# Kernel optimization log

Hardware: AMD Instinct MI355X
Metric: run time of the kernel (lower is better)

Reference implementation:

```python
import jax, jax.numpy as jnp
import numpy as np

B, S, E = 2, 2048, 1024
H = 16
D = E // H          # head_dim = 64
W = 32              # sliding window / block size


def setup_inputs() -> dict:
    key = jax.random.key(0)
    k1, k2, k3 = jax.random.split(key, 3)
    x = jax.random.normal(k1, (B, S, E), dtype=jnp.float32)
    # xavier-uniform-like scale for the projections
    lim_qkv = float(np.sqrt(6.0 / (E + 3 * E)))
    lim_o = float(np.sqrt(6.0 / (E + E)))
    Wqkv = jax.random.uniform(k2, (3 * E, E), minval=-lim_qkv, maxval=lim_qkv, dtype=jnp.float32)
    bqkv = jnp.zeros((3 * E,), dtype=jnp.float32)
    Wo = jax.random.uniform(k3, (E, E), minval=-lim_o, maxval=lim_o, dtype=jnp.float32)
    bo = jnp.zeros((E,), dtype=jnp.float32)
    return {"x": x, "Wqkv": Wqkv, "bqkv": bqkv, "Wo": Wo, "bo": bo}


def _roll_blocks(kb, w):
    # kb: (BH, nb, w, d). Replicates roll(): w circularly-shifted copies along the
    # block axis, original inserted at index (w-1)//2, concatenated within-block.
    shifts = list(range(1, w))
    shifts.insert((w - 1) // 2, 0)
    return jnp.concatenate([jnp.roll(kb, s, axis=1) for s in shifts], axis=2)  # (BH, nb, w*w, d)


def reference(x, Wqkv, bqkv, Wo, bo):
    b, s, e = x.shape
    qkv = x @ Wqkv.T + bqkv                              # (B,S,3E)
    qkv = qkv.reshape(b, s, H, 3 * D).transpose(0, 2, 1, 3)  # (B,H,S,3D)
    q, k, v = jnp.split(qkv, 3, axis=-1)                 # each (B,H,S,D)

    nb = s // W
    qb = q.reshape(b * H, nb, W, D)
    kb = k.reshape(b * H, nb, W, D)
    kblk = _roll_blocks(kb, W)                           # (BH, nb, W*W, D)
    qk = jnp.einsum('bcxd,bcyd->bcxy', qb, kblk)         # (BH, nb, W, W*W)
    attn = qk.reshape(b, H, s, W * W) / jnp.sqrt(jnp.float32(D))
    attn = jax.nn.softmax(attn, axis=-1)
    # Faithful to torch.einsum('ijkl,ijkm->ijkm', attn, v): sum attn over its
    # last axis (==1 after softmax) and broadcast-multiply v.
    vals = attn.sum(axis=-1, keepdims=True) * v          # (B,H,S,D)

    vals = vals.transpose(0, 2, 1, 3).reshape(b, s, e)   # (B,S,E)
    return vals @ Wo.T + bo
```

## Files before the change

kernel.cpp:

```cpp
#include <hip/hip_runtime.h>
#include <hip/hip_bf16.h>
#include <type_traits>

#define MROWS 4096
#define EDIM  1024

typedef __attribute__((ext_vector_type(8))) __bf16 bf16x8;
typedef __attribute__((ext_vector_type(4))) float f32x4;
typedef __attribute__((ext_vector_type(8))) unsigned short ushort8;
typedef __attribute__((ext_vector_type(4))) unsigned short ushort4v;

__device__ __forceinline__ unsigned short f2bf(float f) {
    unsigned u = __builtin_bit_cast(unsigned, f);
    u += 0x7FFFu + ((u >> 16) & 1u);
    return (unsigned short)(u >> 16);
}

__device__ __forceinline__ void async_load16(const void* g, void* l) {
    __builtin_amdgcn_global_load_lds(
        (const __attribute__((address_space(1))) void*)g,
        (__attribute__((address_space(3))) void*)l, 16, 0, 0);
}

template<int N> __device__ __forceinline__ void wait_vmcnt() {
    if constexpr (N == 0)       asm volatile("s_waitcnt vmcnt(0)" ::: "memory");
    else if constexpr (N == 4)  asm volatile("s_waitcnt vmcnt(4)" ::: "memory");
    else if constexpr (N == 6)  asm volatile("s_waitcnt vmcnt(6)" ::: "memory");
    else if constexpr (N == 8)  asm volatile("s_waitcnt vmcnt(8)" ::: "memory");
    else if constexpr (N == 12) asm volatile("s_waitcnt vmcnt(12)" ::: "memory");
    else static_assert(N < 0, "unsupported vmcnt literal");
}

__device__ __forceinline__ void cast8(const float* __restrict__ in,
                                      unsigned short* __restrict__ out, int i) {
    const float4* p = (const float4*)in + (size_t)i * 2;
    float4 a = p[0], b = p[1];
    ushort8 r;
    r[0] = f2bf(a.x); r[1] = f2bf(a.y); r[2] = f2bf(a.z); r[3] = f2bf(a.w);
    r[4] = f2bf(b.x); r[5] = f2bf(b.y); r[6] = f2bf(b.z); r[7] = f2bf(b.w);
    *((ushort8*)out + i) = r;
}

template<bool BIAS, typename OUT_T, int MD, int ND, int KD,
         int BM, int BN, int BK, int NWM, int NWN, int NBUF>
__device__ __forceinline__ void gemm_bt_body(
    const unsigned short* __restrict__ A, const unsigned short* __restrict__ B,
    OUT_T* __restrict__ C, const float* __restrict__ bias, int id,
    unsigned short* sm)
{
    constexpr int THREADS = NWM * NWN * 64;
    constexpr int NBM = MD / BM, NBN = ND / BN, NWG = NBM * NBN;
    constexpr int CPX = NWG / 8;
    constexpr int WTM = BM / NWM, WTN = BN / NWN;
    constexpr int AM = WTM / 16, AN = WTN / 16;
    constexpr int CHUNKS = BK / 8;
    constexpr int RPP = THREADS / CHUNKS;
    constexpr int TILE = (BM + BN) * BK;
    constexpr int L = BM / RPP + BN / RPP;
    constexpr int NIT = KD / BK;
    constexpr int AHEAD = NBUF - 1;
    static_assert(RPP % 8 == 0, "row-phase must be p-invariant for source swizzle");
    static_assert(CHUNKS == 8, "XOR swizzle assumes 8 chunks per row");

    const int t = threadIdx.x;
    const int swz = (id & 7) * CPX + (id >> 3);
    const int bm = swz / NBN, bn = swz % NBN;

    const int lane = t & 63, wave = t >> 6;
    const int wr = wave / NWN, wc = wave % NWN;

    const int rsub = t / CHUNKS;
    const int kb   = (t % CHUNKS) * 8;
    const int kbs  = kb ^ ((rsub & 7) * 8);

    const unsigned short* Ag = A + (size_t)(bm * BM + rsub) * KD + kbs;
    const unsigned short* Bg = B + (size_t)(bn * BN + rsub) * KD + kbs;

    f32x4 acc[AM][AN] = {};

    auto stage = [&](int buf, int k0) {
        unsigned short* As = sm + buf * TILE;
        unsigned short* Bs = As + BM * BK;
        #pragma unroll
        for (int p = 0; p < BM / RPP; ++p)
            async_load16(Ag + (size_t)(p * RPP) * KD + k0, &As[(rsub + p * RPP) * BK + kb]);
        #pragma unroll
        for (int p = 0; p < BN / RPP; ++p)
            async_load16(Bg + (size_t)(p * RPP) * KD + k0, &Bs[(rsub + p * RPP) * BK + kb]);
    };

    auto compute = [&](int buf) {
        const unsigned short* As = sm + buf * TILE;
        const unsigned short* Bs = As + BM * BK;
        #pragma unroll
        for (int ks = 0; ks < BK / 32; ++ks) {
            bf16x8 a[AM], b[AN];
            #pragma unroll
            for (int mi = 0; mi < AM; ++mi) {
                const int ar = wr * WTM + mi * 16 + (lane & 15);
                const int cg = ks * 4 + (lane >> 4);
                a[mi] = *(const bf16x8*)&As[ar * BK + ((cg ^ (ar & 7)) * 8)];
            }
            #pragma unroll
            for (int ni = 0; ni < AN; ++ni) {
                const int br = wc * WTN + ni * 16 + (lane & 15);
                const int cg = ks * 4 + (lane >> 4);
                b[ni] = *(const bf16x8*)&Bs[br * BK + ((cg ^ (br & 7)) * 8)];
            }
            #pragma unroll
            for (int mi = 0; mi < AM; ++mi)
                #pragma unroll
                for (int ni = 0; ni < AN; ++ni)
                    acc[mi][ni] = __builtin_amdgcn_mfma_f32_16x16x32_bf16(
                        b[ni], a[mi], acc[mi][ni], 0, 0, 0);
        }
    };

    #pragma unroll
    for (int p = 0; p < AHEAD; ++p) stage(p, p * BK);

    for (int it = 0; it < NIT; ++it) {
        __builtin_amdgcn_s_barrier();
        if (it + AHEAD < NIT) {
            stage((it + AHEAD) % NBUF, (it + AHEAD) * BK);
            wait_vmcnt<AHEAD * L>();
        } else if (it + 1 < NIT) {
            wait_vmcnt<L>();
        } else {
            wait_vmcnt<0>();
        }
        __builtin_amdgcn_s_barrier();
        compute(it % NBUF);
    }

    const int mrow  = bm * BM + wr * WTM + (lane & 15);
    const int ncol0 = bn * BN + wc * WTN + (lane >> 4) * 4;
    #pragma unroll
    for (int mi = 0; mi < AM; ++mi) {
        const int row = mrow + mi * 16;
        #pragma unroll
        for (int ni = 0; ni < AN; ++ni) {
            const int col = ncol0 + ni * 16;
            f32x4 v = acc[mi][ni];
            if constexpr (BIAS) {
                const f32x4 bv = *(const f32x4*)&bias[col];
                v += bv;
            }
            if constexpr (std::is_same<OUT_T, float>::value) {
                __builtin_nontemporal_store(v, (f32x4*)&C[(size_t)row * ND + col]);
            } else {
                ushort4v r;
                r[0] = f2bf(v[0]); r[1] = f2bf(v[1]);
                r[2] = f2bf(v[2]); r[3] = f2bf(v[3]);
                *(ushort4v*)&C[(size_t)row * ND + col] = r;
            }
        }
    }
}

__global__ __launch_bounds__(256) void prep_w(
    const float* __restrict__ Wqkv, const float* __restrict__ bqkv,
    const float* __restrict__ Wo, const float* __restrict__ bo,
    unsigned short* __restrict__ WvT, unsigned short* __restrict__ wo_bf,
    float* __restrict__ c)
{
    const int blk = blockIdx.x;
    const int t = threadIdx.x;
    if (blk < 256) {
        __shared__ unsigned short tile[64][65];
        const int eBase = (blk & 15) * 64, kBase = (blk >> 4) * 64;
        const int tx = t & 63, ty = t >> 6;
        #pragma unroll
        for (int r = ty; r < 64; r += 4) {
            int k = kBase + r;
            int j = ((k >> 6) * 192) + 128 + (k & 63);
            tile[r][tx] = f2bf(Wqkv[(size_t)j * EDIM + eBase + tx]);
        }
        __syncthreads();
        #pragma unroll
        for (int r = ty; r < 64; r += 4)
            WvT[(size_t)(eBase + r) * EDIM + kBase + tx] = tile[tx][r];
    } else if (blk < 768) {
        cast8(Wo, wo_bf, (blk - 256) * 256 + t);
    } else {
        const int b = blk - 768;
        const int wave = t >> 6, lane = t & 63;
        for (int r = 0; r < 16; ++r) {
            int row = b * 64 + wave * 16 + r;
            float s = 0.f;
            #pragma unroll
            for (int kk = 0; kk < 16; ++kk) {
                int k = kk * 64 + lane;
                int j = kk * 192 + 128 + lane;
                s += Wo[(size_t)row * EDIM + k] * bqkv[j];
            }
            #pragma unroll
            for (int off = 32; off > 0; off >>= 1) s += __shfl_down(s, off);
            if (lane == 0) c[row] = s + bo[row];
        }
    }
}

__global__ __launch_bounds__(256, 2) void gemm1_castx(
    const unsigned short* __restrict__ wo_bf, const unsigned short* __restrict__ wvt,
    unsigned short* __restrict__ m_bf,
    const float* __restrict__ x, unsigned short* __restrict__ x_bf)
{
    __shared__ unsigned short smem[3 * (64 + 64) * 64];
    const int blk = blockIdx.x;
    if (blk < 256) {
        gemm_bt_body<false, unsigned short, EDIM, EDIM, EDIM, 64, 64, 64, 2, 2, 3>(
            wo_bf, wvt, m_bf, nullptr, blk, smem);
    } else {
        cast8(x, x_bf, (blk - 256) * 256 + threadIdx.x);
    }
}

__global__ __launch_bounds__(512, 2) void gemm2(
    const unsigned short* __restrict__ x_bf, const unsigned short* __restrict__ m_bf,
    float* __restrict__ out, const float* __restrict__ cvec)
{
    __shared__ unsigned short smem[2 * (128 + 128) * 64];
    gemm_bt_body<true, float, MROWS, EDIM, EDIM, 128, 128, 64, 2, 4, 2>(
        x_bf, m_bf, out, cvec, blockIdx.x, smem);
}

extern "C" void kernel_launch(void* const* d_in, const int* in_sizes, int n_in,
                              void* d_out, int out_size, void* d_ws, size_t ws_size,
                              hipStream_t stream) {
    const float* x    = (const float*)d_in[0];
    const float* Wqkv = (const float*)d_in[1];
    const float* bqkv = (const float*)d_in[2];
    const float* Wo   = (const float*)d_in[3];
    const float* bo   = (const float*)d_in[4];
    float* out = (float*)d_out;

    char* ws = (char*)d_ws;
    unsigned short* x_bf  = (unsigned short*)(ws);
    unsigned short* wvt   = (unsigned short*)(ws + 8u  * 1024 * 1024);
    unsigned short* wo_bf = (unsigned short*)(ws + 10u * 1024 * 1024);
    unsigned short* m_bf  = (unsigned short*)(ws + 12u * 1024 * 1024);
    float*          cvec  = (float*)(ws + 14u * 1024 * 1024);

    prep_w<<<784, 256, 0, stream>>>(Wqkv, bqkv, Wo, bo, wvt, wo_bf, cvec);
    gemm1_castx<<<2304, 256, 0, stream>>>(wo_bf, wvt, m_bf, x, x_bf);
    gemm2<<<256, 512, 0, stream>>>(x_bf, m_bf, out, cvec);
}
```

Measured before the change: 40.42 us.

## Fuse fp32-to-bf16 cast of x into the second GEMM's A-tile staging

Removes the separate pass that casts x to bf16 and writes it to workspace. The second GEMM now reads fp32 x directly into registers, converts it with packed bf16 conversion instructions, and writes swizzled bf16 into LDS, while B is still staged asynchronously. This saves a round trip of x through global memory and shrinks the first GEMM launch. In exchange, the A loads become register-staged fp32 reads of twice the bytes, with less latency hiding than the async LDS path.

```diff
diff --git a/kernel.cpp b/kernel.cpp
--- a/kernel.cpp
+++ b/kernel.cpp
@@ -9,11 +9,18 @@
 typedef __attribute__((ext_vector_type(4))) float f32x4;
 typedef __attribute__((ext_vector_type(8))) unsigned short ushort8;
 typedef __attribute__((ext_vector_type(4))) unsigned short ushort4v;
+typedef __attribute__((ext_vector_type(4))) unsigned int uint4v;
 
 __device__ __forceinline__ unsigned short f2bf(float f) {
     unsigned u = __builtin_bit_cast(unsigned, f);
     u += 0x7FFFu + ((u >> 16) & 1u);
     return (unsigned short)(u >> 16);
+}
+
+__device__ __forceinline__ unsigned cvt_pk_bf16(float a, float b) {
+    unsigned r;
+    asm("v_cvt_pk_bf16_f32 %0, %1, %2" : "=v"(r) : "v"(a), "v"(b));
+    return r;
 }
 
 __device__ __forceinline__ void async_load16(const void* g, void* l) {
@@ -201,28 +208,124 @@
     }
 }
 
-__global__ __launch_bounds__(256, 2) void gemm1_castx(
+__global__ __launch_bounds__(256, 2) void gemm1k(
     const unsigned short* __restrict__ wo_bf, const unsigned short* __restrict__ wvt,
-    unsigned short* __restrict__ m_bf,
-    const float* __restrict__ x, unsigned short* __restrict__ x_bf)
+    unsigned short* __restrict__ m_bf)
 {
     __shared__ unsigned short smem[3 * (64 + 64) * 64];
-    const int blk = blockIdx.x;
-    if (blk < 256) {
-        gemm_bt_body<false, unsigned short, EDIM, EDIM, EDIM, 64, 64, 64, 2, 2, 3>(
-            wo_bf, wvt, m_bf, nullptr, blk, smem);
-    } else {
-        cast8(x, x_bf, (blk - 256) * 256 + threadIdx.x);
-    }
-}
-
-__global__ __launch_bounds__(512, 2) void gemm2(
-    const unsigned short* __restrict__ x_bf, const unsigned short* __restrict__ m_bf,
+    gemm_bt_body<false, unsigned short, EDIM, EDIM, EDIM, 64, 64, 64, 2, 2, 3>(
+        wo_bf, wvt, m_bf, nullptr, blockIdx.x, smem);
+}
+
+__global__ __launch_bounds__(512, 2) void gemm2f(
+    const float* __restrict__ x, const unsigned short* __restrict__ Bm,
     float* __restrict__ out, const float* __restrict__ cvec)
 {
-    __shared__ unsigned short smem[2 * (128 + 128) * 64];
-    gemm_bt_body<true, float, MROWS, EDIM, EDIM, 128, 128, 64, 2, 4, 2>(
-        x_bf, m_bf, out, cvec, blockIdx.x, smem);
+    constexpr int BM = 128, BN = 128, BK = 64, NIT = EDIM / BK, NBUF = 2;
+    constexpr int NBM = MROWS / BM, NBN = EDIM / BN, NWG = NBM * NBN;
+    constexpr int CPX = NWG / 8;
+    constexpr int TILE = (BM + BN) * BK;
+    __shared__ unsigned short sm[NBUF * TILE];
+
+    const int t = threadIdx.x;
+    const int id = blockIdx.x;
+    const int swz = (id & 7) * CPX + (id >> 3);
+    const int bm = swz / NBN, bn = swz % NBN;
+
+    const int lane = t & 63, wave = t >> 6;
+    const int wr = wave >> 2, wc = wave & 3;
+
+    const int rowA = t >> 2, j = t & 3;
+    const float* Ag = x + (size_t)(bm * BM + rowA) * EDIM + j * 16;
+    const int c0 = ((2 * j)     ^ (rowA & 7)) * 8;
+    const int c1 = ((2 * j + 1) ^ (rowA & 7)) * 8;
+
+    const int rsubB = t >> 3, kbB = (t & 7) * 8;
+    const int kbsB = kbB ^ ((rsubB & 7) * 8);
+    const unsigned short* Bg = Bm + (size_t)(bn * BN + rsubB) * EDIM + kbsB;
+
+    f32x4 acc[4][2] = {};
+    float4 L0, L1, L2, L3;
+
+    auto issueA = [&](int k0) {
+        const float4* p = (const float4*)(Ag + k0);
+        L0 = p[0]; L1 = p[1]; L2 = p[2]; L3 = p[3];
+    };
+    auto stageB = [&](int buf, int k0) {
+        unsigned short* Bs = sm + buf * TILE + BM * BK;
+        #pragma unroll
+        for (int p = 0; p < 2; ++p)
+            async_load16(Bg + (size_t)(p * 64) * EDIM + k0, &Bs[(rsubB + p * 64) * BK + kbB]);
+    };
+    auto writeA = [&](int buf) {
+        unsigned short* As = sm + buf * TILE;
+        uint4v w0, w1;
+        w0[0] = cvt_pk_bf16(L0.x, L0.y); w0[1] = cvt_pk_bf16(L0.z, L0.w);
+        w0[2] = cvt_pk_bf16(L1.x, L1.y); w0[3] = cvt_pk_bf16(L1.z, L1.w);
+        w1[0] = cvt_pk_bf16(L2.x, L2.y); w1[1] = cvt_pk_bf16(L2.z, L2.w);
+        w1[2] = cvt_pk_bf16(L3.x, L3.y); w1[3] = cvt_pk_bf16(L3.z, L3.w);
+        *(uint4v*)&As[rowA * BK + c0] = w0;
+        *(uint4v*)&As[rowA * BK + c1] = w1;
+    };
+    auto compute = [&](int buf) {
+        const unsigned short* As = sm + buf * TILE;
+        const unsigned short* Bs = As + BM * BK;
+        #pragma unroll
+        for (int ks = 0; ks < 2; ++ks) {
+            bf16x8 a[4], b[2];
+            #pragma unroll
+            for (int mi = 0; mi < 4; ++mi) {
+                const int ar = wr * 64 + mi * 16 + (lane & 15);
+                const int cg = ks * 4 + (lane >> 4);
+                a[mi] = *(const bf16x8*)&As[ar * BK + ((cg ^ (ar & 7)) * 8)];
+            }
+            #pragma unroll
+            for (int ni = 0; ni < 2; ++ni) {
+                const int br = wc * 32 + ni * 16 + (lane & 15);
+                const int cg = ks * 4 + (lane >> 4);
+                b[ni] = *(const bf16x8*)&Bs[br * BK + ((cg ^ (br & 7)) * 8)];
+            }
+            #pragma unroll
+            for (int mi = 0; mi < 4; ++mi)
+                #pragma unroll
+                for (int ni = 0; ni < 2; ++ni)
+                    acc[mi][ni] = __builtin_amdgcn_mfma_f32_16x16x32_bf16(
+                        b[ni], a[mi], acc[mi][ni], 0, 0, 0);
+        }
+    };
+
+    issueA(0);
+    stageB(0, 0);
+
+    for (int it = 0; it < NIT; ++it) {
+        __builtin_amdgcn_s_barrier();
+        writeA(it & 1);
+        if (it + 1 < NIT) {
+            issueA((it + 1) * BK);
+            stageB((it & 1) ^ 1, (it + 1) * BK);
+            wait_vmcnt<6>();
+        } else {
+            wait_vmcnt<0>();
+        }
+        asm volatile("s_waitcnt lgkmcnt(0)" ::: "memory");
+        __builtin_amdgcn_s_barrier();
+        compute(it & 1);
+    }
+
+    const int mrow  = bm * BM + wr * 64 + (lane & 15);
+    const int ncol0 = bn * BN + wc * 32 + (lane >> 4) * 4;
+    #pragma unroll
+    for (int mi = 0; mi < 4; ++mi) {
+        const int row = mrow + mi * 16;
+        #pragma unroll
+        for (int ni = 0; ni < 2; ++ni) {
+            const int col = ncol0 + ni * 16;
+            f32x4 v = acc[mi][ni];
+            const f32x4 bv = *(const f32x4*)&cvec[col];
+            v += bv;
+            __builtin_nontemporal_store(v, (f32x4*)&out[(size_t)row * EDIM + col]);
+        }
+    }
 }
 
 extern "C" void kernel_launch(void* const* d_in, const int* in_sizes, int n_in,
@@ -236,13 +339,12 @@
     float* out = (float*)d_out;
 
     char* ws = (char*)d_ws;
-    unsigned short* x_bf  = (unsigned short*)(ws);
-    unsigned short* wvt   = (unsigned short*)(ws + 8u  * 1024 * 1024);
-    unsigned short* wo_bf = (unsigned short*)(ws + 10u * 1024 * 1024);
-    unsigned short* m_bf  = (unsigned short*)(ws + 12u * 1024 * 1024);
-    float*          cvec  = (float*)(ws + 14u * 1024 * 1024);
+    unsigned short* wvt   = (unsigned short*)(ws);
+    unsigned short* wo_bf = (unsigned short*)(ws + 2u * 1024 * 1024);
+    unsigned short* m_bf  = (unsigned short*)(ws + 4u * 1024 * 1024);
+    float*          cvec  = (float*)(ws + 6u * 1024 * 1024);
 
     prep_w<<<784, 256, 0, stream>>>(Wqkv, bqkv, Wo, bo, wvt, wo_bf, cvec);
-    gemm1_castx<<<2304, 256, 0, stream>>>(wo_bf, wvt, m_bf, x, x_bf);
-    gemm2<<<256, 512, 0, stream>>>(x_bf, m_bf, out, cvec);
-}
+    gemm1k<<<256, 256, 0, stream>>>(wo_bf, wvt, m_bf);
+    gemm2f<<<256, 512, 0, stream>>>(x, m_bf, out, cvec);
+}
```

After: 41.72 us. 3.2% more time.
